# Optimization experiments

Hardware: AMD Instinct MI355X
Metric: run time of the kernel (lower is better)

## Reference

```python
import jax, jax.numpy as jnp
import numpy as np

NTYPES = 8
EXCLUDE = [(0, 1), (2, 3)]
NF, NLOC, NNEI = 4, 16384, 128
NALL = 32768


def _build_type_mask(ntypes, exclude):
    ex = set()
    for a, b in exclude:
        ex.add((a, b))
        ex.add((b, a))
    tm = np.ones((ntypes + 1, ntypes + 1), dtype=np.float32)
    for ti, tj in ex:
        tm[tj, ti] = 0.0
    return tm.reshape(-1)  # flattened [(ntypes+1)^2]


def setup_inputs() -> dict:
    key = jax.random.key(0)
    k1, k2 = jax.random.split(key)
    # nlist in [-1, NALL): -1 marks a missing neighbor
    nlist = jax.random.randint(k1, (NF, NLOC, NNEI), -1, NALL, dtype=jnp.int32)
    atype_ext = jax.random.randint(k2, (NF, NALL), 0, NTYPES, dtype=jnp.int32)
    type_mask = jnp.asarray(_build_type_mask(NTYPES, EXCLUDE))
    return {"nlist": nlist, "atype_ext": atype_ext, "type_mask": type_mask, "ntypes": NTYPES}


def reference(nlist, atype_ext, type_mask, ntypes):
    nf, nloc, nnei = nlist.shape
    nall = atype_ext.shape[1]
    # append virtual type `ntypes` used for -1 (padding) neighbors
    ae = jnp.concatenate(
        [atype_ext, jnp.full((nf, 1), ntypes, dtype=atype_ext.dtype)], axis=-1
    )  # [nf, nall+1]
    type_i = atype_ext[:, :nloc] * (ntypes + 1)  # [nf, nloc]
    index = jnp.where(nlist == -1, nall, nlist)  # [nf, nloc, nnei]
    type_j = jnp.take_along_axis(ae, index.reshape(nf, nloc * nnei), axis=1)
    type_j = type_j.reshape(nf, nloc, nnei)
    type_ij = type_i[:, :, None] + type_j  # flat index into type_mask table
    mask = type_mask[type_ij]  # [nf, nloc, nnei]
    return mask
```

## Files before the change

### kernel.cpp

```cpp
#include <hip/hip_runtime.h>

#define NF    4
#define NLOC  16384
#define NNEI  128
#define NALL  32768

#define ELEMS_PER_FRAME (NLOC * NNEI)
#define Q4_PER_FRAME    (ELEMS_PER_FRAME / 4)
#define THREADS 512
#define BLOCKS_PER_FRAME 256
#define ITERS (Q4_PER_FRAME / (BLOCKS_PER_FRAME * THREADS))

__global__ void __launch_bounds__(256) build_colbits(
    const int* __restrict__ atype_ext,
    const float* __restrict__ type_mask,
    const int* __restrict__ ntypes_p,
    unsigned char* __restrict__ ttab)
{
    const int t = blockIdx.x * blockDim.x + threadIdx.x;
    const int ntypes = ntypes_p[0];
    const int np1 = ntypes + 1;

    const int4 v = reinterpret_cast<const int4*>(atype_ext)[t];
    unsigned bx = 0, by = 0, bz = 0, bw = 0;
    for (int i = 0; i < ntypes; ++i) {
        const float* row = type_mask + i * np1;
        bx |= (row[v.x] != 0.0f ? 1u : 0u) << i;
        by |= (row[v.y] != 0.0f ? 1u : 0u) << i;
        bz |= (row[v.z] != 0.0f ? 1u : 0u) << i;
        bw |= (row[v.w] != 0.0f ? 1u : 0u) << i;
    }
    uchar4 b;
    b.x = (unsigned char)bx; b.y = (unsigned char)by;
    b.z = (unsigned char)bz; b.w = (unsigned char)bw;
    reinterpret_cast<uchar4*>(ttab)[t] = b;

    if (t == 0) {
        unsigned bp = 0;
        for (int i = 0; i < ntypes; ++i)
            bp |= (type_mask[i * np1 + ntypes] != 0.0f ? 1u : 0u) << i;
        ttab[(size_t)NF * NALL] = (unsigned char)bp;
    }
}

__global__ void __launch_bounds__(THREADS) pair_exclude_mask_kernel(
    const int* __restrict__ nlist,
    const unsigned char* __restrict__ ttab,
    const int* __restrict__ atype_ext,
    float* __restrict__ out)
{
    __shared__ unsigned char stt[NALL + 4];

    const int f = blockIdx.x / BLOCKS_PER_FRAME;
    const int b = blockIdx.x % BLOCKS_PER_FRAME;

    {
        const uint4* src = reinterpret_cast<const uint4*>(ttab + (size_t)f * NALL);
        uint4* dst = reinterpret_cast<uint4*>(stt);
        #pragma unroll
        for (int k = 0; k < NALL / 16 / THREADS; ++k)
            dst[threadIdx.x + k * THREADS] = src[threadIdx.x + k * THREADS];
        if (threadIdx.x == 0) stt[NALL] = ttab[(size_t)NF * NALL];
    }
    __syncthreads();

    const int* nl_base = nlist + (size_t)f * ELEMS_PER_FRAME;
    float* out_base = out + (size_t)f * ELEMS_PER_FRAME;
    const int* at_base = atype_ext + (size_t)f * NALL;
    const int q0 = b * (THREADS * ITERS);

    const int qA = q0 + 0 * THREADS + threadIdx.x;
    const int qB = q0 + 1 * THREADS + threadIdx.x;
    const int qC = q0 + 2 * THREADS + threadIdx.x;
    const int qD = q0 + 3 * THREADS + threadIdx.x;

    const int4 nlA = reinterpret_cast<const int4*>(nl_base)[qA];
    const int4 nlB = reinterpret_cast<const int4*>(nl_base)[qB];
    const int4 nlC = reinterpret_cast<const int4*>(nl_base)[qC];
    const int4 nlD = reinterpret_cast<const int4*>(nl_base)[qD];
    const int tiA = at_base[qA >> 5];
    const int tiB = at_base[qB >> 5];
    const int tiC = at_base[qC >> 5];
    const int tiD = at_base[qD >> 5];

#define DO4(nl, ti, q)                                                        \
    {                                                                         \
        const unsigned ix = min((unsigned)nl.x, (unsigned)NALL);              \
        const unsigned iy = min((unsigned)nl.y, (unsigned)NALL);              \
        const unsigned iz = min((unsigned)nl.z, (unsigned)NALL);              \
        const unsigned iw = min((unsigned)nl.w, (unsigned)NALL);              \
        float4 m;                                                             \
        m.x = (float)((stt[ix] >> ti) & 1);                                   \
        m.y = (float)((stt[iy] >> ti) & 1);                                   \
        m.z = (float)((stt[iz] >> ti) & 1);                                   \
        m.w = (float)((stt[iw] >> ti) & 1);                                   \
        reinterpret_cast<float4*>(out_base)[q] = m;                           \
    }

    DO4(nlA, tiA, qA)
    DO4(nlB, tiB, qB)
    DO4(nlC, tiC, qC)
    DO4(nlD, tiD, qD)
#undef DO4
}

extern "C" void kernel_launch(void* const* d_in, const int* in_sizes, int n_in,
                              void* d_out, int out_size, void* d_ws, size_t ws_size,
                              hipStream_t stream) {
    const int*   nlist     = (const int*)d_in[0];
    const int*   atype_ext = (const int*)d_in[1];
    const float* type_mask = (const float*)d_in[2];
    const int*   ntypes_p  = (const int*)d_in[3];
    float*       out       = (float*)d_out;
    unsigned char* ttab    = (unsigned char*)d_ws;

    build_colbits<<<(NF * NALL / 4) / 256, 256, 0, stream>>>(
        atype_ext, type_mask, ntypes_p, ttab);

    pair_exclude_mask_kernel<<<NF * BLOCKS_PER_FRAME, THREADS, 0, stream>>>(
        nlist, ttab, atype_ext, out);
}
```

Baseline: 91.91 us.

## Fuse column-bit table build into mask kernel and use nontemporal loads/stores

Removes the separate build_colbits kernel. Each block now builds a small per-type bitmask table in shared memory and converts the frame's atype_ext row into per-atom bit bytes itself, so there is one launch instead of two and no workspace round trip. Each block reads 128KB of int types instead of 32KB of precomputed bytes, which adds redundant L2 traffic across the 256 blocks per frame. The nlist loads and output stores are also made nontemporal to reduce cache pollution on the streaming traffic.

```diff
diff --git a/kernel.cpp b/kernel.cpp
--- a/kernel.cpp
+++ b/kernel.cpp
@@ -11,62 +11,51 @@
 #define BLOCKS_PER_FRAME 256
 #define ITERS (Q4_PER_FRAME / (BLOCKS_PER_FRAME * THREADS))
 
-__global__ void __launch_bounds__(256) build_colbits(
+typedef int   iv4 __attribute__((ext_vector_type(4)));
+typedef float fv4 __attribute__((ext_vector_type(4)));
+
+__global__ void __launch_bounds__(THREADS) pair_exclude_mask_fused(
+    const int* __restrict__ nlist,
     const int* __restrict__ atype_ext,
     const float* __restrict__ type_mask,
     const int* __restrict__ ntypes_p,
-    unsigned char* __restrict__ ttab)
-{
-    const int t = blockIdx.x * blockDim.x + threadIdx.x;
-    const int ntypes = ntypes_p[0];
-    const int np1 = ntypes + 1;
-
-    const int4 v = reinterpret_cast<const int4*>(atype_ext)[t];
-    unsigned bx = 0, by = 0, bz = 0, bw = 0;
-    for (int i = 0; i < ntypes; ++i) {
-        const float* row = type_mask + i * np1;
-        bx |= (row[v.x] != 0.0f ? 1u : 0u) << i;
-        by |= (row[v.y] != 0.0f ? 1u : 0u) << i;
-        bz |= (row[v.z] != 0.0f ? 1u : 0u) << i;
-        bw |= (row[v.w] != 0.0f ? 1u : 0u) << i;
-    }
-    uchar4 b;
-    b.x = (unsigned char)bx; b.y = (unsigned char)by;
-    b.z = (unsigned char)bz; b.w = (unsigned char)bw;
-    reinterpret_cast<uchar4*>(ttab)[t] = b;
-
-    if (t == 0) {
-        unsigned bp = 0;
-        for (int i = 0; i < ntypes; ++i)
-            bp |= (type_mask[i * np1 + ntypes] != 0.0f ? 1u : 0u) << i;
-        ttab[(size_t)NF * NALL] = (unsigned char)bp;
-    }
-}
-
-__global__ void __launch_bounds__(THREADS) pair_exclude_mask_kernel(
-    const int* __restrict__ nlist,
-    const unsigned char* __restrict__ ttab,
-    const int* __restrict__ atype_ext,
     float* __restrict__ out)
 {
     __shared__ unsigned char stt[NALL + 4];
+    __shared__ unsigned char ctab[16];
 
     const int f = blockIdx.x / BLOCKS_PER_FRAME;
     const int b = blockIdx.x % BLOCKS_PER_FRAME;
 
+    const int ntypes = ntypes_p[0];
+    const int np1 = ntypes + 1;
+
+    if (threadIdx.x < (unsigned)np1) {
+        unsigned bits = 0;
+        for (int i = 0; i < ntypes; ++i)
+            bits |= (type_mask[i * np1 + threadIdx.x] != 0.0f ? 1u : 0u) << i;
+        ctab[threadIdx.x] = (unsigned char)bits;
+    }
+    __syncthreads();
+
+    const int* at_base = atype_ext + (size_t)f * NALL;
     {
-        const uint4* src = reinterpret_cast<const uint4*>(ttab + (size_t)f * NALL);
-        uint4* dst = reinterpret_cast<uint4*>(stt);
+        const iv4* src = reinterpret_cast<const iv4*>(at_base);
+        uchar4* dst = reinterpret_cast<uchar4*>(stt);
         #pragma unroll
-        for (int k = 0; k < NALL / 16 / THREADS; ++k)
-            dst[threadIdx.x + k * THREADS] = src[threadIdx.x + k * THREADS];
-        if (threadIdx.x == 0) stt[NALL] = ttab[(size_t)NF * NALL];
+        for (int k = 0; k < NALL / 4 / THREADS; ++k) {
+            const iv4 v = src[threadIdx.x + k * THREADS];
+            uchar4 c;
+            c.x = ctab[v.x]; c.y = ctab[v.y];
+            c.z = ctab[v.z]; c.w = ctab[v.w];
+            dst[threadIdx.x + k * THREADS] = c;
+        }
+        if (threadIdx.x == 0) stt[NALL] = ctab[ntypes];
     }
     __syncthreads();
 
     const int* nl_base = nlist + (size_t)f * ELEMS_PER_FRAME;
     float* out_base = out + (size_t)f * ELEMS_PER_FRAME;
-    const int* at_base = atype_ext + (size_t)f * NALL;
     const int q0 = b * (THREADS * ITERS);
 
     const int qA = q0 + 0 * THREADS + threadIdx.x;
@@ -74,10 +63,10 @@
     const int qC = q0 + 2 * THREADS + threadIdx.x;
     const int qD = q0 + 3 * THREADS + threadIdx.x;
 
-    const int4 nlA = reinterpret_cast<const int4*>(nl_base)[qA];
-    const int4 nlB = reinterpret_cast<const int4*>(nl_base)[qB];
-    const int4 nlC = reinterpret_cast<const int4*>(nl_base)[qC];
-    const int4 nlD = reinterpret_cast<const int4*>(nl_base)[qD];
+    const iv4 nlA = __builtin_nontemporal_load(reinterpret_cast<const iv4*>(nl_base) + qA);
+    const iv4 nlB = __builtin_nontemporal_load(reinterpret_cast<const iv4*>(nl_base) + qB);
+    const iv4 nlC = __builtin_nontemporal_load(reinterpret_cast<const iv4*>(nl_base) + qC);
+    const iv4 nlD = __builtin_nontemporal_load(reinterpret_cast<const iv4*>(nl_base) + qD);
     const int tiA = at_base[qA >> 5];
     const int tiB = at_base[qB >> 5];
     const int tiC = at_base[qC >> 5];
@@ -89,12 +78,12 @@
         const unsigned iy = min((unsigned)nl.y, (unsigned)NALL);              \
         const unsigned iz = min((unsigned)nl.z, (unsigned)NALL);              \
         const unsigned iw = min((unsigned)nl.w, (unsigned)NALL);              \
-        float4 m;                                                             \
-        m.x = (float)((stt[ix] >> ti) & 1);                                   \
-        m.y = (float)((stt[iy] >> ti) & 1);                                   \
-        m.z = (float)((stt[iz] >> ti) & 1);                                   \
-        m.w = (float)((stt[iw] >> ti) & 1);                                   \
-        reinterpret_cast<float4*>(out_base)[q] = m;                           \
+        fv4 m;                                                                \
+        m.x = ((stt[ix] >> ti) & 1) ? 1.0f : 0.0f;                            \
+        m.y = ((stt[iy] >> ti) & 1) ? 1.0f : 0.0f;                            \
+        m.z = ((stt[iz] >> ti) & 1) ? 1.0f : 0.0f;                            \
+        m.w = ((stt[iw] >> ti) & 1) ? 1.0f : 0.0f;                            \
+        __builtin_nontemporal_store(m, reinterpret_cast<fv4*>(out_base) + q); \
     }
 
     DO4(nlA, tiA, qA)
@@ -112,11 +101,7 @@
     const float* type_mask = (const float*)d_in[2];
     const int*   ntypes_p  = (const int*)d_in[3];
     float*       out       = (float*)d_out;
-    unsigned char* ttab    = (unsigned char*)d_ws;
 
-    build_colbits<<<(NF * NALL / 4) / 256, 256, 0, stream>>>(
-        atype_ext, type_mask, ntypes_p, ttab);
-
-    pair_exclude_mask_kernel<<<NF * BLOCKS_PER_FRAME, THREADS, 0, stream>>>(
-        nlist, ttab, atype_ext, out);
+    pair_exclude_mask_fused<<<NF * BLOCKS_PER_FRAME, THREADS, 0, stream>>>(
+        nlist, atype_ext, type_mask, ntypes_p, out);
 }
```

After: 97.29 us. 5.9% more time.
